# Kernel optimization log

Hardware: AMD Instinct MI355X
Metric: run time of the kernel (lower is better)

Reference implementation:

```python
import jax, jax.numpy as jnp
import numpy as np

KS, STRIDE, PAD, GROUPS = 7, 1, 3, 8


def setup_inputs() -> dict:
    key = jax.random.key(0)
    ks = jax.random.split(key, 6)
    B, C, H, W = 4, 128, 64, 64
    O = 128
    rel_size = O // GROUPS // 2  # 8
    return {
        "x": jax.random.normal(ks[0], (B, C, H, W), jnp.float32),
        "wq": jax.random.normal(ks[1], (O, C), jnp.float32) * 0.05,
        "wk": jax.random.normal(ks[2], (O, C), jnp.float32) * 0.05,
        "wv": jax.random.normal(ks[3], (O, C), jnp.float32) * 0.05,
        "rel_x": jax.random.normal(ks[4], (rel_size, KS), jnp.float32),
        "rel_y": jax.random.normal(ks[5], (O // GROUPS - rel_size, KS), jnp.float32),
    }


def _patches(a, fH, fW):
    # a: [B, C, pH, pW] -> [B, C, fH, fW, KS, KS] (overlapping windows, like torch unfold)
    cols = []
    for ki in range(KS):
        rows = []
        for kj in range(KS):
            rows.append(a[:, :, ki:ki + (fH - 1) * STRIDE + 1:STRIDE,
                             kj:kj + (fW - 1) * STRIDE + 1:STRIDE])
        cols.append(jnp.stack(rows, axis=-1))  # last axis = l (W-kernel)
    return jnp.stack(cols, axis=-2)            # second-to-last = k (H-kernel)


def reference(x, wq, wk, wv, rel_x, rel_y):
    B, C, H, W = x.shape
    O = wq.shape[0]
    rel_size = rel_x.shape[0]
    xp = jnp.pad(x, ((0, 0), (0, 0), (PAD, PAD), (PAD, PAD)))
    pH, pW = H + 2 * PAD, W + 2 * PAD
    fH, fW = (pH - KS) // STRIDE + 1, (pW - KS) // STRIDE + 1
    # 1x1 convs
    q = jnp.einsum('oc,bchw->bohw', wq, xp)
    k = jnp.einsum('oc,bchw->bohw', wk, xp)
    v = jnp.einsum('oc,bchw->bohw', wv, xp)
    h0 = (KS - 1) // 2
    win_q = q[:, :, h0:pH - KS // 2:STRIDE, h0:pW - KS // 2:STRIDE]  # [B,O,fH,fW]
    win_q_b = win_q.reshape(B, GROUPS, O // GROUPS, fH, fW)
    qx = win_q_b[:, :, :rel_size]
    qy = win_q_b[:, :, rel_size:]
    bias_x = jnp.einsum('bgxhw,xk->bhwk', qx, rel_x)  # varies along l (W-kernel)
    bias_y = jnp.einsum('bgyhw,yk->bhwk', qy, rel_y)  # varies along k (H-kernel)
    win_k = _patches(k, fH, fW)  # [B,O,fH,fW,KS,KS]
    win_v = _patches(v, fH, fW)
    logits = jnp.einsum('bchw,bchwkl->bhwkl', win_q, win_k)
    logits = logits + bias_x[:, :, :, None, :] + bias_y[:, :, :, :, None]
    attn = jax.nn.softmax(logits.reshape(B, fH, fW, KS * KS), axis=-1)
    attn = attn.reshape(B, fH, fW, KS, KS)
    out = jnp.einsum('bhwkl,bchwkl->bchw', attn, win_v)  # [B,O,fH,fW]
    return out
```

## Files before the change

### kernel.cpp

```cpp
#include <hip/hip_runtime.h>

typedef __fp16 half8_t __attribute__((ext_vector_type(8)));
typedef float  f4_t    __attribute__((ext_vector_type(4)));

__device__ __forceinline__ unsigned pk(float a, float b) {
    return __builtin_bit_cast(unsigned, __builtin_amdgcn_cvt_pkrtz(a, b));
}

__global__ __launch_bounds__(256) void qkv_fused(
    const float* __restrict__ x, const float* __restrict__ wq,
    const float* __restrict__ wk, const float* __restrict__ wv,
    const float* __restrict__ relx, const float* __restrict__ rely,
    unsigned* __restrict__ qf, unsigned* __restrict__ kf,
    unsigned* __restrict__ vf, float* __restrict__ biasG)
{
    __shared__ __fp16 Af[2048 * 8];
    __shared__ float  tl4[4][16 * 17];
    __shared__ float  sS[4][16 * 20];
    __shared__ float  relsQ[120];

    const int tid = threadIdx.x, wvn = tid >> 6, lane = tid & 63;
    const int mtx = blockIdx.x >> 8;
    const int tg  = blockIdx.x & 255;
    const float* wsrc = (mtx == 0) ? wq : (mtx == 1 ? wk : wv);
    unsigned*    dst  = (mtx == 0) ? qf : (mtx == 1 ? kf : vf);

    if (tid < 120)
        relsQ[tid] = (tid < 56) ? relx[tid] : (tid < 112 ? rely[tid - 56] : 0.f);

#pragma unroll
    for (int s = 0; s < 8; ++s) {
        const int it = s * 256 + tid;
        const int l = it & 63, ck = (it >> 6) & 3, ot = it >> 8;
        const float* wr = wsrc + (size_t)(ot * 16 + (l & 15)) * 128 + ck * 32 + (l >> 4) * 8;
        const float4 w0 = *(const float4*)wr;
        const float4 w1 = *(const float4*)(wr + 4);
        unsigned* d = (unsigned*)&Af[it * 8];
        d[0] = pk(w0.x, w0.y); d[1] = pk(w0.z, w0.w);
        d[2] = pk(w1.x, w1.y); d[3] = pk(w1.z, w1.w);
    }

    const int t = tg * 4 + wvn;
    const int m = lane & 15, quad = lane >> 4;
    const int p0 = t * 16, b = p0 >> 12, hw = p0 & 4095;
    const float* xb = x + (size_t)b * (128 * 4096) + hw + m;
    half8_t B[4];
#pragma unroll
    for (int ck = 0; ck < 4; ++ck) {
        float f[8];
#pragma unroll
        for (int j = 0; j < 8; ++j) f[j] = xb[(size_t)(ck * 32 + quad * 8 + j) * 4096];
        unsigned* d = (unsigned*)&B[ck];
        d[0] = pk(f[0], f[1]); d[1] = pk(f[2], f[3]);
        d[2] = pk(f[4], f[5]); d[3] = pk(f[6], f[7]);
    }
    __syncthreads();

    float* tl = tl4[wvn];
    float s0 = 0.f, s1 = 0.f, s2 = 0.f, s3 = 0.f;
#pragma unroll
    for (int og = 0; og < 4; ++og) {
#pragma unroll
        for (int ot = 0; ot < 2; ++ot) {
            const int otile = og * 2 + ot;
            f4_t acc = {0.f, 0.f, 0.f, 0.f};
#pragma unroll
            for (int ck = 0; ck < 4; ++ck) {
                const half8_t A = *(const half8_t*)&Af[((otile * 4 + ck) * 64 + lane) * 8];
                acc = __builtin_amdgcn_mfma_f32_16x16x32_f16(A, B[ck], acc, 0, 0, 0);
            }
            if (mtx == 0) { s0 += acc[0]; s1 += acc[1]; s2 += acc[2]; s3 += acc[3]; }
            const int c2l = ot * 8 + quad * 2;
            tl[m * 17 + c2l]     = __builtin_bit_cast(float, pk(acc[0], acc[1]));
            tl[m * 17 + c2l + 1] = __builtin_bit_cast(float, pk(acc[2], acc[3]));
        }
        __asm__ volatile("s_waitcnt lgkmcnt(0)" ::: "memory");
        __builtin_amdgcn_wave_barrier();
#pragma unroll
        for (int s = 0; s < 4; ++s) {
            const int px = s * 4 + quad;
            dst[(size_t)(p0 + px) * 64 + og * 16 + m] =
                __builtin_bit_cast(unsigned, tl[px * 17 + m]);
        }
        __builtin_amdgcn_wave_barrier();
    }

    if (mtx == 0) {
        f4_t sv = {s0, s1, s2, s3};
        *(f4_t*)&sS[wvn][m * 20 + quad * 4] = sv;
        __asm__ volatile("s_waitcnt lgkmcnt(0)" ::: "memory");
        __builtin_amdgcn_wave_barrier();
        f4_t bj = {0.f, 0.f, 0.f, 0.f};
#pragma unroll
        for (int jj = 0; jj < 4; ++jj) {
            const int j = quad * 4 + jj;
            float s = 0.f;
            if (j < 7) {
#pragma unroll
                for (int tt = 0; tt < 8; ++tt)
                    s = fmaf(sS[wvn][m * 20 + tt], relsQ[tt * 7 + j], s);
            } else if (j < 14) {
#pragma unroll
                for (int tt = 0; tt < 8; ++tt)
                    s = fmaf(sS[wvn][m * 20 + 8 + tt], relsQ[56 + tt * 7 + (j - 7)], s);
            }
            bj[jj] = s;
        }
        *(f4_t*)(biasG + (size_t)(p0 + m) * 16 + quad * 4) = bj;
    }
}

__global__ __launch_bounds__(256) void attn_mfma(
    const unsigned* __restrict__ qf, const unsigned* __restrict__ kf,
    const unsigned* __restrict__ vf, const float* __restrict__ biasG,
    float* __restrict__ out)
{
    __shared__ __fp16 vH[128 * 216];
    __shared__ __fp16 aW[4 * 16 * 136];
    __shared__ float  biasL[64 * 17];

    const int tid = threadIdx.x, bx = blockIdx.x;
    const int wv = tid >> 6, lane = tid & 63;
    const int n = lane & 15, quad = lane >> 4;
    const int w0 = (bx & 7) * 8, h0 = ((bx >> 3) & 7) * 8, b = bx >> 6;

    for (int i = tid; i < 1568; i += 256) {
        const int pq = i >> 5, c2p = i & 31;
        const int pos0 = pq * 4;
        unsigned dx[4], dy[4];
#pragma unroll
        for (int p = 0; p < 4; ++p) {
            const int pos = pos0 + p;
            const int ri = (pos * 2341) >> 15;
            const int ci = pos - ri * 14;
            const int py = h0 - 3 + ri, px = w0 - 3 + ci;
            uint2 d = make_uint2(0u, 0u);
            if ((unsigned)py < 64u && (unsigned)px < 64u)
                d = *(const uint2*)(vf + (size_t)((b * 4096 + py * 64 + px) * 64 + c2p * 2));
            dx[p] = d.x; dy[p] = d.y;
        }
        const int c0 = c2p * 4;
        *(uint2*)(vH + (c0 + 0) * 216 + pos0) = make_uint2(
            __builtin_amdgcn_perm(dx[1], dx[0], 0x05040100u),
            __builtin_amdgcn_perm(dx[3], dx[2], 0x05040100u));
        *(uint2*)(vH + (c0 + 1) * 216 + pos0) = make_uint2(
            __builtin_amdgcn_perm(dx[1], dx[0], 0x07060302u),
            __builtin_amdgcn_perm(dx[3], dx[2], 0x07060302u));
        *(uint2*)(vH + (c0 + 2) * 216 + pos0) = make_uint2(
            __builtin_amdgcn_perm(dy[1], dy[0], 0x05040100u),
            __builtin_amdgcn_perm(dy[3], dy[2], 0x05040100u));
        *(uint2*)(vH + (c0 + 3) * 216 + pos0) = make_uint2(
            __builtin_amdgcn_perm(dy[1], dy[0], 0x07060302u),
            __builtin_amdgcn_perm(dy[3], dy[2], 0x07060302u));
    }
    for (int i = tid; i < 640; i += 256) {
        const int c = i / 5, s = i - c * 5;
        *(uint2*)(vH + c * 216 + 196 + s * 4) = make_uint2(0u, 0u);
    }
    for (int i = tid; i < 1024; i += 256) {
        const int px = i >> 4, tt = i & 15;
        const int pix = b * 4096 + (h0 + (px >> 3)) * 64 + w0 + (px & 7);
        biasL[px * 17 + tt] = biasG[(size_t)pix * 16 + tt];
    }
    __syncthreads();

    const int wrow = h0 + wv * 2;
    uint4 qA[4];
#pragma unroll
    for (int kc = 0; kc < 4; ++kc) {
        const int pix = b * 4096 + (wrow + (n >> 3)) * 64 + w0 + (n & 7);
        qA[kc] = *(const uint4*)(qf + (size_t)pix * 64 + kc * 16 + quad * 4);
    }
    f4_t lg[7];
#pragma unroll
    for (int t = 0; t < 7; ++t) {
        const int posL = t * 16 + n;
        const int ri = (posL * 2341) >> 15;
        const int ci = posL - ri * 14;
        const int py = wrow - 3 + ri, pxc = w0 - 3 + ci;
        const bool val = ((unsigned)py < 64u) && ((unsigned)pxc < 64u);
        const int pix = b * 4096 + py * 64 + pxc;
        f4_t acc = {0.f, 0.f, 0.f, 0.f};
#pragma unroll
        for (int kc = 0; kc < 4; ++kc) {
            uint4 kB = make_uint4(0u, 0u, 0u, 0u);
            if (val) kB = *(const uint4*)(kf + (size_t)pix * 64 + kc * 16 + quad * 4);
            acc = __builtin_amdgcn_mfma_f32_16x16x32_f16(
                __builtin_bit_cast(half8_t, qA[kc]),
                __builtin_bit_cast(half8_t, kB), acc, 0, 0, 0);
        }
        lg[t] = acc;
    }

    const int pad = (wv & 1) * 4;
    {
        const int row = lane >> 2, ch = lane & 3;
        const int off = pad ? (ch == 0 ? 0 : 112 + pad + (ch - 1) * 4)
                            : 112 + ch * 4;
        *(uint2*)(aW + wv * 2176 + row * 136 + off) = make_uint2(0u, 0u);
    }
#pragma unroll
    for (int i = 0; i < 4; ++i) {
        const int px = quad * 4 + i;
        const int dr = px >> 3, dw = px & 7;
        const float* bb = &biasL[(wv * 16 + px) * 17];
        float mx = -1e30f;
#pragma unroll
        for (int t = 0; t < 7; ++t) {
            const int posL = t * 16 + n;
            const int ri = (posL * 2341) >> 15;
            const int ci = posL - ri * 14;
            const unsigned ki = ri - dr, kj = ci - dw;
            float v = -1e30f;
            if (ki < 7u && kj < 7u) v = lg[t][i] + bb[kj] + bb[7 + ki];
            lg[t][i] = v;
            mx = fmaxf(mx, v);
        }
        mx = fmaxf(mx, __shfl_xor(mx, 1));
        mx = fmaxf(mx, __shfl_xor(mx, 2));
        mx = fmaxf(mx, __shfl_xor(mx, 4));
        mx = fmaxf(mx, __shfl_xor(mx, 8));
        float ss = 0.f;
#pragma unroll
        for (int t = 0; t < 7; ++t) {
            const float e = __expf(lg[t][i] - mx);
            lg[t][i] = e;
            ss += e;
        }
        ss += __shfl_xor(ss, 1);
        ss += __shfl_xor(ss, 2);
        ss += __shfl_xor(ss, 4);
        ss += __shfl_xor(ss, 8);
        const float inv = 1.f / ss;
#pragma unroll
        for (int t = 0; t < 7; ++t)
            aW[wv * 2176 + px * 136 + pad + t * 16 + n] = (__fp16)(lg[t][i] * inv);
    }
    __asm__ volatile("s_waitcnt lgkmcnt(0)" ::: "memory");
    __builtin_amdgcn_wave_barrier();

    const int startw = wv * 28 - pad;
    uint4 pA[4];
#pragma unroll
    for (int kc = 0; kc < 4; ++kc)
        pA[kc] = *(const uint4*)(aW + wv * 2176 + n * 136 + kc * 32 + quad * 8);
#pragma unroll
    for (int tn = 0; tn < 8; ++tn) {
        f4_t acc = {0.f, 0.f, 0.f, 0.f};
#pragma unroll
        for (int kc = 0; kc < 4; ++kc) {
            const half8_t vB = *(const half8_t*)(vH + (tn * 16 + n) * 216 +
                                                 startw + kc * 32 + quad * 8);
            acc = __builtin_amdgcn_mfma_f32_16x16x32_f16(
                __builtin_bit_cast(half8_t, pA[kc]), vB, acc, 0, 0, 0);
        }
        const int c = tn * 16 + n;
#pragma unroll
        for (int i = 0; i < 4; ++i) {
            const int px = quad * 4 + i;
            const int hwp = (wrow + (px >> 3)) * 64 + w0 + (px & 7);
            out[(size_t)(b * 128 + c) * 4096 + hwp] = acc[i];
        }
    }
}

extern "C" void kernel_launch(void* const* d_in, const int* in_sizes, int n_in,
                              void* d_out, int out_size, void* d_ws, size_t ws_size,
                              hipStream_t stream) {
    const float* x    = (const float*)d_in[0];
    const float* wq   = (const float*)d_in[1];
    const float* wk   = (const float*)d_in[2];
    const float* wv   = (const float*)d_in[3];
    const float* relx = (const float*)d_in[4];
    const float* rely = (const float*)d_in[5];
    float* out = (float*)d_out;

    char* ws = (char*)d_ws;
    unsigned* qfb = (unsigned*)(ws);
    unsigned* kfb = (unsigned*)(ws + 0x400000);
    unsigned* vfb = (unsigned*)(ws + 0x800000);
    float*    bG  = (float*)   (ws + 0xC00000);

    qkv_fused<<<dim3(768), 256, 0, stream>>>(x, wq, wk, wv, relx, rely,
                                             qfb, kfb, vfb, bG);
    attn_mfma<<<dim3(256), 256, 0, stream>>>(qfb, kfb, vfb, bG, out);
}
```

Measured before the change: 97.41 us.

## Shrink attention tile to 4x8 pixels, one query row per wave, smaller LDS

The attention kernel now gives each block a 4-row by 8-column output tile, doubling the grid to 512 blocks. Each wave handles one query row, so the key window maps directly onto 7 rows by 16 columns without the divide-by-14 index math. The V tile and bias buffers shrink, the QKV kernel reuses one shared buffer for its transpose and bias scratch, and it gains a min-blocks launch bound to raise occupancy. The cost is more halo reloading of V and K per output pixel, half-empty MFMA rows in the QK stage, and an extra block-wide barrier before the PV stage.

```diff
diff --git a/kernel.cpp b/kernel.cpp
--- a/kernel.cpp
+++ b/kernel.cpp
@@ -7,7 +7,7 @@
     return __builtin_bit_cast(unsigned, __builtin_amdgcn_cvt_pkrtz(a, b));
 }
 
-__global__ __launch_bounds__(256) void qkv_fused(
+__global__ __launch_bounds__(256, 4) void qkv_fused(
     const float* __restrict__ x, const float* __restrict__ wq,
     const float* __restrict__ wk, const float* __restrict__ wv,
     const float* __restrict__ relx, const float* __restrict__ rely,
@@ -15,8 +15,7 @@
     unsigned* __restrict__ vf, float* __restrict__ biasG)
 {
     __shared__ __fp16 Af[2048 * 8];
-    __shared__ float  tl4[4][16 * 17];
-    __shared__ float  sS[4][16 * 20];
+    __shared__ float  uB[4][320];
     __shared__ float  relsQ[120];
 
     const int tid = threadIdx.x, wvn = tid >> 6, lane = tid & 63;
@@ -56,7 +55,7 @@
     }
     __syncthreads();
 
-    float* tl = tl4[wvn];
+    float* tl = uB[wvn];
     float s0 = 0.f, s1 = 0.f, s2 = 0.f, s3 = 0.f;
 #pragma unroll
     for (int og = 0; og < 4; ++og) {
@@ -86,8 +85,11 @@
     }
 
     if (mtx == 0) {
+        float* sS = uB[wvn];
         f4_t sv = {s0, s1, s2, s3};
-        *(f4_t*)&sS[wvn][m * 20 + quad * 4] = sv;
+        __asm__ volatile("s_waitcnt lgkmcnt(0)" ::: "memory");
+        __builtin_amdgcn_wave_barrier();
+        *(f4_t*)&sS[m * 20 + quad * 4] = sv;
         __asm__ volatile("s_waitcnt lgkmcnt(0)" ::: "memory");
         __builtin_amdgcn_wave_barrier();
         f4_t bj = {0.f, 0.f, 0.f, 0.f};
@@ -98,93 +100,102 @@
             if (j < 7) {
 #pragma unroll
                 for (int tt = 0; tt < 8; ++tt)
-                    s = fmaf(sS[wvn][m * 20 + tt], relsQ[tt * 7 + j], s);
+                    s = fmaf(sS[m * 20 + tt], relsQ[tt * 7 + j], s);
             } else if (j < 14) {
 #pragma unroll
                 for (int tt = 0; tt < 8; ++tt)
-                    s = fmaf(sS[wvn][m * 20 + 8 + tt], relsQ[56 + tt * 7 + (j - 7)], s);
+                    s = fmaf(sS[m * 20 + 8 + tt], relsQ[56 + tt * 7 + (j - 7)], s);
             }
             bj[jj] = s;
         }
         *(f4_t*)(biasG + (size_t)(p0 + m) * 16 + quad * 4) = bj;
     }
 }
+
+constexpr int VP = 168;
 
 __global__ __launch_bounds__(256) void attn_mfma(
     const unsigned* __restrict__ qf, const unsigned* __restrict__ kf,
     const unsigned* __restrict__ vf, const float* __restrict__ biasG,
     float* __restrict__ out)
 {
-    __shared__ __fp16 vH[128 * 216];
-    __shared__ __fp16 aW[4 * 16 * 136];
-    __shared__ float  biasL[64 * 17];
+    __shared__ __fp16 vH[128 * VP];
+    __shared__ __fp16 aW[2][16 * 136];
+    __shared__ float  biasL[32 * 16];
 
     const int tid = threadIdx.x, bx = blockIdx.x;
     const int wv = tid >> 6, lane = tid & 63;
-    const int n = lane & 15, quad = lane >> 4;
-    const int w0 = (bx & 7) * 8, h0 = ((bx >> 3) & 7) * 8, b = bx >> 6;
-
-    for (int i = tid; i < 1568; i += 256) {
-        const int pq = i >> 5, c2p = i & 31;
-        const int pos0 = pq * 4;
-        unsigned dx[4], dy[4];
-#pragma unroll
-        for (int p = 0; p < 4; ++p) {
-            const int pos = pos0 + p;
-            const int ri = (pos * 2341) >> 15;
-            const int ci = pos - ri * 14;
-            const int py = h0 - 3 + ri, px = w0 - 3 + ci;
-            uint2 d = make_uint2(0u, 0u);
-            if ((unsigned)py < 64u && (unsigned)px < 64u)
-                d = *(const uint2*)(vf + (size_t)((b * 4096 + py * 64 + px) * 64 + c2p * 2));
-            dx[p] = d.x; dy[p] = d.y;
-        }
-        const int c0 = c2p * 4;
-        *(uint2*)(vH + (c0 + 0) * 216 + pos0) = make_uint2(
-            __builtin_amdgcn_perm(dx[1], dx[0], 0x05040100u),
-            __builtin_amdgcn_perm(dx[3], dx[2], 0x05040100u));
-        *(uint2*)(vH + (c0 + 1) * 216 + pos0) = make_uint2(
-            __builtin_amdgcn_perm(dx[1], dx[0], 0x07060302u),
-            __builtin_amdgcn_perm(dx[3], dx[2], 0x07060302u));
-        *(uint2*)(vH + (c0 + 2) * 216 + pos0) = make_uint2(
-            __builtin_amdgcn_perm(dy[1], dy[0], 0x05040100u),
-            __builtin_amdgcn_perm(dy[3], dy[2], 0x05040100u));
-        *(uint2*)(vH + (c0 + 3) * 216 + pos0) = make_uint2(
-            __builtin_amdgcn_perm(dy[1], dy[0], 0x07060302u),
-            __builtin_amdgcn_perm(dy[3], dy[2], 0x07060302u));
-    }
-    for (int i = tid; i < 640; i += 256) {
-        const int c = i / 5, s = i - c * 5;
-        *(uint2*)(vH + c * 216 + 196 + s * 4) = make_uint2(0u, 0u);
-    }
-    for (int i = tid; i < 1024; i += 256) {
+    const int w0 = (bx & 7) * 8;
+    const int h0 = ((bx >> 3) & 15) * 4;
+    const int b  = bx >> 7;
+    const int s  = wv >> 1, u = wv & 1;
+    const int wr = h0 + 2 * s + u;
+    const int n16 = lane & 15, quad = lane >> 4;
+
+    for (int i = tid; i < 2176; i += 256) ((unsigned*)aW)[i] = 0u;
+
+    {
+        const int g = tid >> 3, r = tid & 7;
+#pragma unroll
+        for (int it = 0; it < 5; ++it) {
+            const int pq = r + 8 * it;
+            const int hi = pq >> 2, ciq = pq & 3;
+            const int py = h0 - 3 + hi;
+            unsigned d0[4], d1[4];
+#pragma unroll
+            for (int p = 0; p < 4; ++p) {
+                const int pxc = w0 - 3 + ciq * 4 + p;
+                uint2 d = make_uint2(0u, 0u);
+                if ((unsigned)py < 64u && (unsigned)pxc < 64u)
+                    d = *(const uint2*)(vf + (size_t)((b * 4096 + py * 64 + pxc) * 64 + g * 2));
+                d0[p] = d.x; d1[p] = d.y;
+            }
+            const int c0 = g * 4, off = hi * 16 + ciq * 4;
+            *(uint2*)(vH + (c0 + 0) * VP + off) = make_uint2(
+                __builtin_amdgcn_perm(d0[1], d0[0], 0x05040100u),
+                __builtin_amdgcn_perm(d0[3], d0[2], 0x05040100u));
+            *(uint2*)(vH + (c0 + 1) * VP + off) = make_uint2(
+                __builtin_amdgcn_perm(d0[1], d0[0], 0x07060302u),
+                __builtin_amdgcn_perm(d0[3], d0[2], 0x07060302u));
+            *(uint2*)(vH + (c0 + 2) * VP + off) = make_uint2(
+                __builtin_amdgcn_perm(d1[1], d1[0], 0x05040100u),
+                __builtin_amdgcn_perm(d1[3], d1[2], 0x05040100u));
+            *(uint2*)(vH + (c0 + 3) * VP + off) = make_uint2(
+                __builtin_amdgcn_perm(d1[1], d1[0], 0x07060302u),
+                __builtin_amdgcn_perm(d1[3], d1[2], 0x07060302u));
+        }
+    }
+
+    for (int i = tid; i < 512; i += 256) {
         const int px = i >> 4, tt = i & 15;
         const int pix = b * 4096 + (h0 + (px >> 3)) * 64 + w0 + (px & 7);
-        biasL[px * 17 + tt] = biasG[(size_t)pix * 16 + tt];
+        biasL[px * 16 + tt] = biasG[(size_t)pix * 16 + tt];
     }
     __syncthreads();
 
-    const int wrow = h0 + wv * 2;
     uint4 qA[4];
-#pragma unroll
-    for (int kc = 0; kc < 4; ++kc) {
-        const int pix = b * 4096 + (wrow + (n >> 3)) * 64 + w0 + (n & 7);
-        qA[kc] = *(const uint4*)(qf + (size_t)pix * 64 + kc * 16 + quad * 4);
+    {
+        const bool vm = n16 < 8;
+        const size_t qb = (size_t)(b * 4096 + wr * 64 + w0 + n16) * 64;
+#pragma unroll
+        for (int kc = 0; kc < 4; ++kc) {
+            uint4 t4 = make_uint4(0u, 0u, 0u, 0u);
+            if (vm) t4 = *(const uint4*)(qf + qb + kc * 16 + quad * 4);
+            qA[kc] = t4;
+        }
     }
     f4_t lg[7];
 #pragma unroll
     for (int t = 0; t < 7; ++t) {
-        const int posL = t * 16 + n;
-        const int ri = (posL * 2341) >> 15;
-        const int ci = posL - ri * 14;
-        const int py = wrow - 3 + ri, pxc = w0 - 3 + ci;
+        const int py = wr - 3 + t;
+        const int pxc = w0 - 3 + n16;
         const bool val = ((unsigned)py < 64u) && ((unsigned)pxc < 64u);
-        const int pix = b * 4096 + py * 64 + pxc;
+        const size_t kb = (size_t)(b * 4096 + py * 64 + pxc) * 64;
         f4_t acc = {0.f, 0.f, 0.f, 0.f};
 #pragma unroll
         for (int kc = 0; kc < 4; ++kc) {
             uint4 kB = make_uint4(0u, 0u, 0u, 0u);
-            if (val) kB = *(const uint4*)(kf + (size_t)pix * 64 + kc * 16 + quad * 4);
+            if (val) kB = *(const uint4*)(kf + kb + kc * 16 + quad * 4);
             acc = __builtin_amdgcn_mfma_f32_16x16x32_f16(
                 __builtin_bit_cast(half8_t, qA[kc]),
                 __builtin_bit_cast(half8_t, kB), acc, 0, 0, 0);
@@ -192,28 +203,20 @@
         lg[t] = acc;
     }
 
-    const int pad = (wv & 1) * 4;
-    {
-        const int row = lane >> 2, ch = lane & 3;
-        const int off = pad ? (ch == 0 ? 0 : 112 + pad + (ch - 1) * 4)
-                            : 112 + ch * 4;
-        *(uint2*)(aW + wv * 2176 + row * 136 + off) = make_uint2(0u, 0u);
-    }
+    const int rowblk = 2 * s + u;
 #pragma unroll
     for (int i = 0; i < 4; ++i) {
-        const int px = quad * 4 + i;
-        const int dr = px >> 3, dw = px & 7;
-        const float* bb = &biasL[(wv * 16 + px) * 17];
+        const int m = quad * 4 + i;
+        const float* bb = &biasL[(rowblk * 8 + (m & 7)) * 16];
+        const int kj = n16 - m;
+        const bool kv = (unsigned)kj < 7u;
+        const float bx2 = kv ? bb[kj] : 0.f;
+        float lv[7];
         float mx = -1e30f;
 #pragma unroll
         for (int t = 0; t < 7; ++t) {
-            const int posL = t * 16 + n;
-            const int ri = (posL * 2341) >> 15;
-            const int ci = posL - ri * 14;
-            const unsigned ki = ri - dr, kj = ci - dw;
-            float v = -1e30f;
-            if (ki < 7u && kj < 7u) v = lg[t][i] + bb[kj] + bb[7 + ki];
-            lg[t][i] = v;
+            const float v = kv ? lg[t][i] + bx2 + bb[7 + t] : -1e30f;
+            lv[t] = v;
             mx = fmaxf(mx, v);
         }
         mx = fmaxf(mx, __shfl_xor(mx, 1));
@@ -223,8 +226,8 @@
         float ss = 0.f;
 #pragma unroll
         for (int t = 0; t < 7; ++t) {
-            const float e = __expf(lg[t][i] - mx);
-            lg[t][i] = e;
+            const float e = __expf(lv[t] - mx);
+            lv[t] = e;
             ss += e;
         }
         ss += __shfl_xor(ss, 1);
@@ -232,34 +235,38 @@
         ss += __shfl_xor(ss, 4);
         ss += __shfl_xor(ss, 8);
         const float inv = 1.f / ss;
-#pragma unroll
-        for (int t = 0; t < 7; ++t)
-            aW[wv * 2176 + px * 136 + pad + t * 16 + n] = (__fp16)(lg[t][i] * inv);
-    }
-    __asm__ volatile("s_waitcnt lgkmcnt(0)" ::: "memory");
-    __builtin_amdgcn_wave_barrier();
-
-    const int startw = wv * 28 - pad;
+        if (m < 8) {
+            __fp16* wp = &aW[s][(u * 8 + m) * 136];
+#pragma unroll
+            for (int t = 0; t < 7; ++t)
+                wp[(u + t) * 16 + n16] = (__fp16)(lv[t] * inv);
+        }
+    }
+    __syncthreads();
+
     uint4 pA[4];
 #pragma unroll
     for (int kc = 0; kc < 4; ++kc)
-        pA[kc] = *(const uint4*)(aW + wv * 2176 + n * 136 + kc * 32 + quad * 8);
-#pragma unroll
-    for (int tn = 0; tn < 8; ++tn) {
+        pA[kc] = *(const uint4*)(&aW[s][n16 * 136 + kc * 32 + quad * 8]);
+#pragma unroll
+    for (int tt = 0; tt < 4; ++tt) {
+        const int tn = u * 4 + tt;
         f4_t acc = {0.f, 0.f, 0.f, 0.f};
 #pragma unroll
         for (int kc = 0; kc < 4; ++kc) {
-            const half8_t vB = *(const half8_t*)(vH + (tn * 16 + n) * 216 +
-                                                 startw + kc * 32 + quad * 8);
+            const int kri = kc * 2 + (quad >> 1);
+            const int ci0 = (quad & 1) * 8;
+            const half8_t vB = *(const half8_t*)(
+                vH + (tn * 16 + n16) * VP + (2 * s + kri) * 16 + ci0);
             acc = __builtin_amdgcn_mfma_f32_16x16x32_f16(
                 __builtin_bit_cast(half8_t, pA[kc]), vB, acc, 0, 0, 0);
         }
-        const int c = tn * 16 + n;
+        const int c = tn * 16 + n16;
+        float* ob = out + (size_t)(b * 128 + c) * 4096;
 #pragma unroll
         for (int i = 0; i < 4; ++i) {
-            const int px = quad * 4 + i;
-            const int hwp = (wrow + (px >> 3)) * 64 + w0 + (px & 7);
-            out[(size_t)(b * 128 + c) * 4096 + hwp] = acc[i];
+            const int mm = quad * 4 + i;
+            ob[(h0 + 2 * s + (mm >> 3)) * 64 + w0 + (mm & 7)] = acc[i];
         }
     }
 }
@@ -283,5 +290,5 @@
 
     qkv_fused<<<dim3(768), 256, 0, stream>>>(x, wq, wk, wv, relx, rely,
                                              qfb, kfb, vfb, bG);
-    attn_mfma<<<dim3(256), 256, 0, stream>>>(qfb, kfb, vfb, bG, out);
-}
+    attn_mfma<<<dim3(512), 256, 0, stream>>>(qfb, kfb, vfb, bG, out);
+}
```

Result: no change. 98.50 us (+1.1%).
